# Performance work log

Hardware: AMD Instinct MI355X
Metric: run time of the kernel (lower is better)

Reference implementation:

```python
import jax, jax.numpy as jnp
import numpy as np

N_NODES = 50000
N_EDGES = 600000
IN_C = 128
HID = 128
OUT_C = 64
N_GCN = 4  # num_layers - 2
SKIP = 0.5
EPS = 1e-5


def setup_inputs() -> dict:
    key = jax.random.key(0)
    ks = jax.random.split(key, 10)
    x = jax.random.normal(ks[0], (N_NODES, IN_C), dtype=jnp.float32)
    edge_index = jax.random.randint(ks[1], (2, N_EDGES), 0, N_NODES, dtype=jnp.int64)
    s = 0.05
    W_in = jax.random.normal(ks[2], (IN_C, HID), dtype=jnp.float32) * s
    b_in = jnp.zeros((HID,), jnp.float32)
    W_g = jax.random.normal(ks[3], (N_GCN, HID, HID), dtype=jnp.float32) * s
    b_g = jnp.zeros((N_GCN, HID), jnp.float32)
    gamma = jnp.ones((N_GCN, HID), jnp.float32)
    beta = jnp.zeros((N_GCN, HID), jnp.float32)
    W_out = jax.random.normal(ks[4], (HID, OUT_C), dtype=jnp.float32) * s
    b_out = jnp.zeros((OUT_C,), jnp.float32)
    return {"x": x, "W_in": W_in, "b_in": b_in, "W_g": W_g, "b_g": b_g,
            "gamma": gamma, "beta": beta, "W_out": W_out, "b_out": b_out,
            "edge_index": edge_index}


def _forward(x, W_in, b_in, W_g, b_g, gamma, beta, W_out, b_out, edge_index):
    n = x.shape[0]
    src, dst = edge_index[0], edge_index[1]
    # GCN symmetric normalization with self-loops: deg = in-degree + 1
    deg = jnp.zeros((n,), x.dtype).at[dst].add(1.0) + 1.0
    dis = jax.lax.rsqrt(deg)  # deg >= 1 thanks to self-loops
    enorm = dis[src] * dis[dst]        # [E] per-edge norm
    self_norm = dis * dis              # [N] self-loop norm

    h = x @ W_in + b_in                # convs[0]: Linear in->hidden
    x_skip = h
    acc = jnp.zeros_like(h)
    for i in range(W_g.shape[0]):      # GCNConv layers (original i = 1..num_layers-2)
        t = h @ W_g[i]                 # [N, HID]
        agg = jax.ops.segment_sum(t[src] * enorm[:, None], dst, num_segments=n)
        agg = agg + t * self_norm[:, None] + b_g[i]  # self-loops + GCNConv bias
        # BatchNorm1d (training-mode batch stats, biased variance)
        mean = agg.mean(axis=0)
        var = jnp.mean((agg - mean) ** 2, axis=0)
        t = (agg - mean) * jax.lax.rsqrt(var + EPS) * gamma[i] + beta[i]
        if (i + 1) % 2 == 0:           # original: if i % 2 == 0 with i starting at 1
            t = t + SKIP * x_skip
        h = jax.nn.relu(t)             # dropout = identity (eval mode)
        acc = acc + h
    return acc @ W_out + b_out         # convs[-1]: Linear hidden->out


def reference(x, W_in, b_in, W_g, b_g, gamma, beta, W_out, b_out, edge_index):
    return _forward(x, W_in, b_in, W_g, b_g, gamma, beta, W_out, b_out, edge_index)
```

## Files before the change

kernel.cpp:

```cpp
#include <hip/hip_runtime.h>

using short8  = __attribute__((ext_vector_type(8))) short;
using floatx4 = __attribute__((ext_vector_type(4))) float;

static __device__ __forceinline__ float bf2f(unsigned short u) {
    union { unsigned u; float f; } v; v.u = ((unsigned)u) << 16; return v.f;
}
static __device__ __forceinline__ unsigned short f2bf(float f) {
    union { float f; unsigned u; } v; v.f = f;
    unsigned r = v.u + 0x7FFFu + ((v.u >> 16) & 1u);
    return (unsigned short)(r >> 16);
}

__global__ void histw_kernel(const int* __restrict__ dst, int* __restrict__ cnt, int E,
                             const float* __restrict__ Win, const float* __restrict__ Wg,
                             const float* __restrict__ Wout,
                             unsigned short* __restrict__ WinT, unsigned short* __restrict__ WgT,
                             unsigned short* __restrict__ WoutT) {
    int HB = (E + 255) >> 8;
    int b = blockIdx.x;
    if (b < HB) {
        int i = b * 256 + threadIdx.x;
        if (i < E) atomicAdd(&cnt[dst[i]], 1);
    } else {
        int i = (b - HB) * 256 + threadIdx.x;
        if (i < 16384) {
            int m = i & 127, k = i >> 7;
            WinT[m * 128 + k] = f2bf(Win[i]);
        } else if (i < 81920) {
            int j = i - 16384;
            int m = j & 127, k = (j >> 7) & 127, mat = j >> 14;
            WgT[mat * 16384 + m * 128 + k] = f2bf(Wg[j]);
        } else if (i < 90112) {
            int j = i - 81920;
            int m = j % 64, k = j / 64;
            WoutT[m * 128 + k] = f2bf(Wout[j]);
        }
    }
}

__global__ __launch_bounds__(256) void scanall_kernel(const int* __restrict__ cnt,
        unsigned* __restrict__ bsum, unsigned* __restrict__ boff, unsigned* __restrict__ done,
        int* __restrict__ rowptr, int* __restrict__ cursor,
        float* __restrict__ dis, float* __restrict__ selfn, int n, int nb) {
    __shared__ int s[256];
    __shared__ int s2[256];
    __shared__ int flag_agg;
    __shared__ int blkoff;
    const int b = blockIdx.x, tid = threadIdx.x;
    int i = b * 256 + tid;
    int cc = (i < n) ? cnt[i] : 0;
    s[tid] = cc;
    __syncthreads();
    for (int off = 1; off < 256; off <<= 1) {
        int t = s[tid];
        int a = (tid >= off) ? s[tid - off] : 0;
        __syncthreads();
        s[tid] = t + a;
        __syncthreads();
    }
    if (tid == 0) {
        atomicExch(&bsum[b], (unsigned)s[255] | 0x80000000u);
        __threadfence();
        unsigned t = atomicAdd(done, 1u);
        flag_agg = (t == (unsigned)(nb - 1)) ? 1 : 0;
    }
    __syncthreads();
    if (flag_agg) {
        __threadfence();
        unsigned val = (tid < nb) ? (atomicOr(&bsum[tid], 0u) & 0x7fffffffu) : 0u;
        s2[tid] = (int)val;
        __syncthreads();
        for (int off = 1; off < 256; off <<= 1) {
            int t = s2[tid];
            int a = (tid >= off) ? s2[tid - off] : 0;
            __syncthreads();
            s2[tid] = t + a;
            __syncthreads();
        }
        if (tid < nb)
            atomicExch(&boff[tid], ((unsigned)s2[tid] - val) | 0x80000000u);
    }
    if (tid == 0) {
        unsigned vv;
        while (((vv = atomicOr(&boff[b], 0u)) & 0x80000000u) == 0u)
            __builtin_amdgcn_s_sleep(8);
        blkoff = (int)(vv & 0x7fffffffu);
    }
    __syncthreads();
    if (i < n) {
        int pre = blkoff + s[tid] - cc;
        rowptr[i] = pre;
        cursor[i] = pre;
        float d = (float)cc + 1.0f;
        dis[i] = rsqrtf(d);
        selfn[i] = 1.0f / d;
        if (i == n - 1) rowptr[n] = pre + cc;
    }
}

__global__ __launch_bounds__(256) void fillgemm_kernel(
        const float* __restrict__ X,
        const unsigned short* __restrict__ W1T, const float* __restrict__ b1,
        const unsigned short* __restrict__ W2T,
        unsigned short* __restrict__ H0, unsigned short* __restrict__ T0, int nrows, int GB,
        const int* __restrict__ src, const int* __restrict__ dst,
        int* __restrict__ cursor, const float* __restrict__ dis,
        unsigned long long* __restrict__ epack, int E) {
    __shared__ unsigned short Al[64 * 136];
    __shared__ unsigned short Wl[128 * 136];
    const int tid = threadIdx.x;

    if (blockIdx.x >= GB) {
        int i = (blockIdx.x - GB) * 256 + tid;
        if (i < E) {
            int s = src[i], d = dst[i];
            int p = atomicAdd(&cursor[d], 1);
            float w = dis[s] * dis[d];
            unsigned long long rec = (unsigned long long)(unsigned)s |
                                     ((unsigned long long)__float_as_uint(w) << 32);
            __builtin_nontemporal_store(rec, &epack[p]);
        }
        return;
    }

    const int w     = tid >> 6;
    const int lane  = tid & 63;
    const int col_l = lane & 15;
    const int quad  = lane >> 4;
    const int row_base = blockIdx.x * 64;

#pragma unroll
    for (int it = 0; it < 8; ++it) {
        int idx = it * 256 + tid;
        int r = idx >> 5, c4 = idx & 31;
        int gr = row_base + r; if (gr >= nrows) gr = nrows - 1;
        float4 v = *(const float4*)&X[(size_t)gr * 128 + c4 * 4];
        ushort4 u;
        u.x = f2bf(v.x); u.y = f2bf(v.y); u.z = f2bf(v.z); u.w = f2bf(v.w);
        *(ushort4*)&Al[r * 136 + c4 * 4] = u;
    }
#pragma unroll
    for (int it = 0; it < 8; ++it) {
        int idx = it * 256 + tid;
        int r = idx >> 4, ch = idx & 15;
        *(float4*)&Wl[r * 136 + ch * 8] = *(const float4*)&W1T[(size_t)r * 128 + ch * 8];
    }
    __syncthreads();

    short8 af[4];
    const int arow = w * 16 + col_l;
#pragma unroll
    for (int ks = 0; ks < 4; ++ks)
        af[ks] = *(const short8*)&Al[arow * 136 + ks * 32 + quad * 8];

    floatx4 acc[8];
#pragma unroll
    for (int ct = 0; ct < 8; ++ct) {
        acc[ct] = (floatx4){0.f, 0.f, 0.f, 0.f};
#pragma unroll
        for (int ks = 0; ks < 4; ++ks) {
            short8 bf = *(const short8*)&Wl[(ct * 16 + col_l) * 136 + ks * 32 + quad * 8];
            acc[ct] = __builtin_amdgcn_mfma_f32_16x16x32_bf16(af[ks], bf, acc[ct], 0, 0, 0);
        }
    }
    __syncthreads();

#pragma unroll
    for (int ct = 0; ct < 8; ++ct) {
        int col = ct * 16 + col_l;
        float bv = b1[col];
#pragma unroll
        for (int r = 0; r < 4; ++r) {
            int row_l = w * 16 + quad * 4 + r;
            float o = acc[ct][r] + bv;
            unsigned short ob = f2bf(o);
            Al[row_l * 136 + col] = ob;
            int gr = row_base + row_l;
            if (gr < nrows) H0[(size_t)gr * 128 + col] = ob;
        }
    }
#pragma unroll
    for (int it = 0; it < 8; ++it) {
        int idx = it * 256 + tid;
        int r = idx >> 4, ch = idx & 15;
        *(float4*)&Wl[r * 136 + ch * 8] = *(const float4*)&W2T[(size_t)r * 128 + ch * 8];
    }
    __syncthreads();

#pragma unroll
    for (int ks = 0; ks < 4; ++ks)
        af[ks] = *(const short8*)&Al[arow * 136 + ks * 32 + quad * 8];
#pragma unroll
    for (int ct = 0; ct < 8; ++ct) {
        acc[ct] = (floatx4){0.f, 0.f, 0.f, 0.f};
#pragma unroll
        for (int ks = 0; ks < 4; ++ks) {
            short8 bf = *(const short8*)&Wl[(ct * 16 + col_l) * 136 + ks * 32 + quad * 8];
            acc[ct] = __builtin_amdgcn_mfma_f32_16x16x32_bf16(af[ks], bf, acc[ct], 0, 0, 0);
        }
    }
#pragma unroll
    for (int ct = 0; ct < 8; ++ct) {
        int col = ct * 16 + col_l;
#pragma unroll
        for (int r = 0; r < 4; ++r) {
            int gr = row_base + w * 16 + quad * 4 + r;
            if (gr < nrows) T0[(size_t)gr * 128 + col] = f2bf(acc[ct][r]);
        }
    }
}

template<int MO, bool STAGE_ACC, bool OB16>
__global__ __launch_bounds__(256) void mgemm_bn_kernel(
        const unsigned short* __restrict__ AGGB, const float* __restrict__ stats,
        const float* __restrict__ gamma, const float* __restrict__ beta,
        const unsigned short* __restrict__ XSKIP, unsigned short* __restrict__ ACC,
        const unsigned short* __restrict__ WT, const float* __restrict__ bias,
        void* __restrict__ C, int nrows, float inv_n, int do_skip, int first) {
    constexpr int NT = MO / 16;
    __shared__ unsigned short Al[64 * 136];
    __shared__ unsigned short Wl[MO * 136];
    __shared__ float ABl[256];
    const int tid   = threadIdx.x;
    const int w     = tid >> 6;
    const int lane  = tid & 63;
    const int col_l = lane & 15;
    const int quad  = lane >> 4;
    const int row_base = blockIdx.x * 64;

    if (tid < 128) {
        float s = 0.f, ss = 0.f;
#pragma unroll
        for (int k = 0; k < 8; ++k) {
            s  += stats[k * 256 + tid];
            ss += stats[k * 256 + 128 + tid];
        }
        float m = s * inv_n;
        float var = ss * inv_n - m * m;
        float inv = rsqrtf(var + 1e-5f);
        float Ax = inv * gamma[tid];
        ABl[tid] = Ax;
        ABl[128 + tid] = beta[tid] - m * Ax;
    }
#pragma unroll
    for (int it = 0; it < MO / 16; ++it) {
        int idx = it * 256 + tid;
        int r = idx >> 4, ch = idx & 15;
        *(float4*)&Wl[r * 136 + ch * 8] = *(const float4*)&WT[(size_t)r * 128 + ch * 8];
    }
    __syncthreads();

#pragma unroll
    for (int it = 0; it < 8; ++it) {
        int idx = it * 256 + tid;
        int r = idx >> 5, c4 = idx & 31;
        int gr = row_base + r;
        ushort4 hu = make_ushort4(0, 0, 0, 0);
        if (gr < nrows) {
            ushort4 xb = *(const ushort4*)&AGGB[(size_t)gr * 128 + c4 * 4];
            float4 Av = ((const float4*)ABl)[c4];
            float4 Bv = ((const float4*)ABl)[32 + c4];
            float4 t;
            t.x = fmaf(bf2f(xb.x), Av.x, Bv.x);
            t.y = fmaf(bf2f(xb.y), Av.y, Bv.y);
            t.z = fmaf(bf2f(xb.z), Av.z, Bv.z);
            t.w = fmaf(bf2f(xb.w), Av.w, Bv.w);
            if (do_skip) {
                ushort4 sk = *(const ushort4*)&XSKIP[(size_t)gr * 128 + c4 * 4];
                t.x = fmaf(0.5f, bf2f(sk.x), t.x);
                t.y = fmaf(0.5f, bf2f(sk.y), t.y);
                t.z = fmaf(0.5f, bf2f(sk.z), t.z);
                t.w = fmaf(0.5f, bf2f(sk.w), t.w);
            }
            t.x = fmaxf(t.x, 0.f); t.y = fmaxf(t.y, 0.f);
            t.z = fmaxf(t.z, 0.f); t.w = fmaxf(t.w, 0.f);
            float4 a;
            if (first) {
                a = t;
            } else {
                ushort4 ab = *(const ushort4*)&ACC[(size_t)gr * 128 + c4 * 4];
                a.x = bf2f(ab.x) + t.x;
                a.y = bf2f(ab.y) + t.y;
                a.z = bf2f(ab.z) + t.z;
                a.w = bf2f(ab.w) + t.w;
            }
            float4 sv;
            if (STAGE_ACC) sv = a; else sv = t;
            hu.x = f2bf(sv.x); hu.y = f2bf(sv.y); hu.z = f2bf(sv.z); hu.w = f2bf(sv.w);
            if (!STAGE_ACC) {
                ushort4 au;
                au.x = f2bf(a.x); au.y = f2bf(a.y); au.z = f2bf(a.z); au.w = f2bf(a.w);
                *(ushort4*)&ACC[(size_t)gr * 128 + c4 * 4] = au;
            }
        }
        *(ushort4*)&Al[r * 136 + c4 * 4] = hu;
    }
    __syncthreads();

    short8 af[4];
    const int arow = w * 16 + col_l;
#pragma unroll
    for (int ks = 0; ks < 4; ++ks)
        af[ks] = *(const short8*)&Al[arow * 136 + ks * 32 + quad * 8];

    floatx4 acc[NT];
#pragma unroll
    for (int ct = 0; ct < NT; ++ct) {
        acc[ct] = (floatx4){0.f, 0.f, 0.f, 0.f};
#pragma unroll
        for (int ks = 0; ks < 4; ++ks) {
            short8 bf = *(const short8*)&Wl[(ct * 16 + col_l) * 136 + ks * 32 + quad * 8];
            acc[ct] = __builtin_amdgcn_mfma_f32_16x16x32_bf16(af[ks], bf, acc[ct], 0, 0, 0);
        }
    }

#pragma unroll
    for (int ct = 0; ct < NT; ++ct) {
        int col = ct * 16 + col_l;
        float bv = bias ? bias[col] : 0.f;
#pragma unroll
        for (int r = 0; r < 4; ++r) {
            int gr = row_base + w * 16 + quad * 4 + r;
            if (gr < nrows) {
                float o = acc[ct][r] + bv;
                if (OB16) ((unsigned short*)C)[(size_t)gr * MO + col] = f2bf(o);
                else      ((float*)C)[(size_t)gr * MO + col] = o;
            }
        }
    }
}

__global__ __launch_bounds__(256) void aggstat_kernel(const unsigned short* __restrict__ T,
        const int* __restrict__ rowptr, const unsigned long long* __restrict__ epack,
        const float* __restrict__ selfn,
        unsigned short* __restrict__ AGGB, float* __restrict__ stats, int n, int nw) {
    const int w    = threadIdx.x >> 6;
    const int lane = threadIdx.x & 63;
    const int wid  = blockIdx.x * 4 + w;
    const int c    = lane * 2;
    float s1x = 0.f, s1y = 0.f, s2x = 0.f, s2y = 0.f;

    for (int v = wid; v < n; v += nw) {
        ushort2 tv = *(const ushort2*)&T[(size_t)v * 128 + c];
        float sn = selfn[v];
        float ax = bf2f(tv.x) * sn, ay = bf2f(tv.y) * sn;
        int e = rowptr[v], e1 = rowptr[v + 1];
        for (; e + 8 <= e1; e += 8) {
            unsigned long long d[8]; ushort2 t[8];
#pragma unroll
            for (int j = 0; j < 8; ++j) d[j] = __builtin_nontemporal_load(&epack[e + j]);
#pragma unroll
            for (int j = 0; j < 8; ++j)
                t[j] = *(const ushort2*)&T[(size_t)(unsigned)d[j] * 128 + c];
#pragma unroll
            for (int j = 0; j < 8; ++j) {
                float wj = __uint_as_float((unsigned)(d[j] >> 32));
                ax = fmaf(wj, bf2f(t[j].x), ax);
                ay = fmaf(wj, bf2f(t[j].y), ay);
            }
        }
        for (; e + 4 <= e1; e += 4) {
            unsigned long long d[4]; ushort2 t[4];
#pragma unroll
            for (int j = 0; j < 4; ++j) d[j] = __builtin_nontemporal_load(&epack[e + j]);
#pragma unroll
            for (int j = 0; j < 4; ++j)
                t[j] = *(const ushort2*)&T[(size_t)(unsigned)d[j] * 128 + c];
#pragma unroll
            for (int j = 0; j < 4; ++j) {
                float wj = __uint_as_float((unsigned)(d[j] >> 32));
                ax = fmaf(wj, bf2f(t[j].x), ax);
                ay = fmaf(wj, bf2f(t[j].y), ay);
            }
        }
        for (; e < e1; ++e) {
            unsigned long long d0 = __builtin_nontemporal_load(&epack[e]);
            ushort2 tu = *(const ushort2*)&T[(size_t)(unsigned)d0 * 128 + c];
            float w0 = __uint_as_float((unsigned)(d0 >> 32));
            ax = fmaf(w0, bf2f(tu.x), ax);
            ay = fmaf(w0, bf2f(tu.y), ay);
        }
        ushort2 o; o.x = f2bf(ax); o.y = f2bf(ay);
        *(ushort2*)&AGGB[(size_t)v * 128 + c] = o;
        float rx = bf2f(o.x), ry = bf2f(o.y);
        s1x += rx; s1y += ry;
        s2x = fmaf(rx, rx, s2x); s2y = fmaf(ry, ry, s2y);
    }

    __shared__ float r1[4][130];
    __shared__ float r2[4][130];
    r1[w][c] = s1x; r1[w][c + 1] = s1y;
    r2[w][c] = s2x; r2[w][c + 1] = s2y;
    __syncthreads();
    if (w == 0) {
        float a1 = r1[0][c] + r1[1][c] + r1[2][c] + r1[3][c];
        float b1 = r1[0][c + 1] + r1[1][c + 1] + r1[2][c + 1] + r1[3][c + 1];
        float a2 = r2[0][c] + r2[1][c] + r2[2][c] + r2[3][c];
        float b2 = r2[0][c + 1] + r2[1][c + 1] + r2[2][c + 1] + r2[3][c + 1];
        float* sh = stats + (blockIdx.x & 7) * 256;
        atomicAdd(&sh[c], a1);
        atomicAdd(&sh[c + 1], b1);
        atomicAdd(&sh[128 + c], a2);
        atomicAdd(&sh[128 + c + 1], b2);
    }
}

extern "C" void kernel_launch(void* const* d_in, const int* in_sizes, int n_in,
                              void* d_out, int out_size, void* d_ws, size_t ws_size,
                              hipStream_t stream) {
    (void)n_in; (void)out_size; (void)ws_size;
    const float* x    = (const float*)d_in[0];
    const float* Win  = (const float*)d_in[1];
    const float* bin  = (const float*)d_in[2];
    const float* Wg   = (const float*)d_in[3];
    const float* gamma = (const float*)d_in[5];
    const float* beta  = (const float*)d_in[6];
    const float* Wout  = (const float*)d_in[7];
    const float* bout  = (const float*)d_in[8];
    const int*   eidx  = (const int*)d_in[9];
    float* out = (float*)d_out;

    const int N = in_sizes[0] / 128;
    const int E = in_sizes[9] / 2;
    const int* esrc_in = eidx;
    const int* edst_in = eidx + E;

    char* p = (char*)d_ws;
    auto alloc = [&](size_t bytes) { char* r = p; p += (bytes + 255) & ~(size_t)255; return r; };
    const size_t NB2 = (size_t)N * 128 * sizeof(unsigned short);
    unsigned short* h0b   = (unsigned short*)alloc(NB2);
    unsigned short* tb16  = (unsigned short*)alloc(NB2);
    unsigned short* aggb  = (unsigned short*)alloc(NB2);
    unsigned short* accb  = (unsigned short*)alloc(NB2);
    unsigned short* WinT  = (unsigned short*)alloc(128 * 128 * 2);
    unsigned short* WgT   = (unsigned short*)alloc(4 * 128 * 128 * 2);
    unsigned short* WoutT = (unsigned short*)alloc(128 * 64 * 2);
    float* disb  = (float*)alloc((size_t)N * 4);
    float* selfn = (float*)alloc((size_t)N * 4);
    char* z0 = p;
    int*      cnt    = (int*)alloc((size_t)N * 4);
    unsigned* bsum   = (unsigned*)alloc(256 * 4);
    unsigned* boff   = (unsigned*)alloc(256 * 4);
    unsigned* done   = (unsigned*)alloc(256);
    float*    stats4 = (float*)alloc((size_t)4 * 8 * 256 * 4);
    const size_t zbytes = (size_t)(p - z0);
    int*   rowptr = (int*)alloc((size_t)(N + 1) * 4);
    int*   cursor = (int*)alloc((size_t)N * 4);
    unsigned long long* epack = (unsigned long long*)alloc((size_t)E * 8);

    auto cdiv = [](int a, int b) { return (a + b - 1) / b; };
    const int NBLK = cdiv(N, 256);
    const float inv_n = 1.0f / (float)N;
    const int AGG_BLOCKS = 2048;
    const int AGG_WAVES  = AGG_BLOCKS * 4;
    const int GB = cdiv(N, 64);
    const int FB = cdiv(E, 256);

    hipMemsetAsync(z0, 0, zbytes, stream);
    histw_kernel<<<cdiv(E, 256) + 352, 256, 0, stream>>>(edst_in, cnt, E,
                                                         Win, Wg, Wout, WinT, WgT, WoutT);
    scanall_kernel<<<NBLK, 256, 0, stream>>>(cnt, bsum, boff, done, rowptr, cursor,
                                             disb, selfn, N, NBLK);

    fillgemm_kernel<<<GB + FB, 256, 0, stream>>>(x, WinT, bin, WgT, h0b, tb16, N, GB,
                                                 esrc_in, edst_in, cursor, disb, epack, E);

    for (int i = 0; i < 4; ++i) {
        float* stats = stats4 + (size_t)i * 8 * 256;
        aggstat_kernel<<<AGG_BLOCKS, 256, 0, stream>>>(tb16, rowptr, epack, selfn,
                                                       aggb, stats, N, AGG_WAVES);
        if (i < 3) {
            mgemm_bn_kernel<128, false, true><<<cdiv(N, 64), 256, 0, stream>>>(
                aggb, stats, gamma + i * 128, beta + i * 128, h0b, accb,
                WgT + (size_t)(i + 1) * 128 * 128, nullptr, (void*)tb16, N,
                inv_n, (i & 1), (i == 0) ? 1 : 0);
        } else {
            mgemm_bn_kernel<64, true, false><<<cdiv(N, 64), 256, 0, stream>>>(
                aggb, stats, gamma + i * 128, beta + i * 128, h0b, accb,
                WoutT, bout, (void*)out, N, inv_n, 1, 0);
        }
    }
}
```

Measured before the change: 417.4 us.

## Build CSR edge list via two-level bucketed staging with shared-memory atomics

```diff
diff --git a/kernel.cpp b/kernel.cpp
--- a/kernel.cpp
+++ b/kernel.cpp
@@ -41,7 +41,7 @@
 
 __global__ __launch_bounds__(256) void scanall_kernel(const int* __restrict__ cnt,
         unsigned* __restrict__ bsum, unsigned* __restrict__ boff, unsigned* __restrict__ done,
-        int* __restrict__ rowptr, int* __restrict__ cursor,
+        int* __restrict__ rowptr,
         float* __restrict__ dis, float* __restrict__ selfn, int n, int nb) {
     __shared__ int s[256];
     __shared__ int s2[256];
@@ -91,7 +91,6 @@
     if (i < n) {
         int pre = blkoff + s[tid] - cc;
         rowptr[i] = pre;
-        cursor[i] = pre;
         float d = (float)cc + 1.0f;
         dis[i] = rsqrtf(d);
         selfn[i] = 1.0f / d;
@@ -105,21 +104,21 @@
         const unsigned short* __restrict__ W2T,
         unsigned short* __restrict__ H0, unsigned short* __restrict__ T0, int nrows, int GB,
         const int* __restrict__ src, const int* __restrict__ dst,
-        int* __restrict__ cursor, const float* __restrict__ dis,
-        unsigned long long* __restrict__ epack, int E) {
+        int* __restrict__ cursor8, unsigned* __restrict__ stage, int E) {
     __shared__ unsigned short Al[64 * 136];
     __shared__ unsigned short Wl[128 * 136];
     const int tid = threadIdx.x;
 
     if (blockIdx.x >= GB) {
-        int i = (blockIdx.x - GB) * 256 + tid;
+        int k = blockIdx.x - GB;
+        int i = k * 256 + tid;
         if (i < E) {
             int s = src[i], d = dst[i];
-            int p = atomicAdd(&cursor[d], 1);
-            float w = dis[s] * dis[d];
-            unsigned long long rec = (unsigned long long)(unsigned)s |
-                                     ((unsigned long long)__float_as_uint(w) << 32);
-            __builtin_nontemporal_store(rec, &epack[p]);
+            int bk = (d >> 8) * 8 + (k & 7);
+            int idx = atomicAdd(&cursor8[bk], 1);
+            if (idx > 1023) idx = 1023;
+            unsigned rec = (unsigned)s | ((unsigned)(d & 255) << 16);
+            __builtin_nontemporal_store(rec, &stage[(unsigned)bk * 1024 + idx]);
         }
         return;
     }
@@ -207,6 +206,35 @@
         for (int r = 0; r < 4; ++r) {
             int gr = row_base + w * 16 + quad * 4 + r;
             if (gr < nrows) T0[(size_t)gr * 128 + col] = f2bf(acc[ct][r]);
+        }
+    }
+}
+
+__global__ __launch_bounds__(256) void scatter_kernel(
+        const unsigned* __restrict__ stage, const int* __restrict__ cursor8,
+        const int* __restrict__ rowptr, const float* __restrict__ dis,
+        unsigned long long* __restrict__ epack, int n) {
+    __shared__ int   curs[256];
+    __shared__ float disn[256];
+    const int b = blockIdx.x, tid = threadIdx.x;
+    int node = b * 256 + tid;
+    if (node < n) { curs[tid] = rowptr[node]; disn[tid] = dis[node]; }
+    else          { curs[tid] = 0;            disn[tid] = 0.f; }
+    __syncthreads();
+#pragma unroll 1
+    for (int s = 0; s < 8; ++s) {
+        int bk  = b * 8 + s;
+        int cnt = cursor8[bk]; if (cnt > 1024) cnt = 1024;
+        const unsigned* sg = stage + (unsigned)bk * 1024;
+        for (int i = tid; i < cnt; i += 256) {
+            unsigned rec = sg[i];
+            int sc = rec & 0xFFFF;
+            int dl = (rec >> 16) & 255;
+            int slot = atomicAdd(&curs[dl], 1);
+            float w = dis[sc] * disn[dl];
+            unsigned long long r2 = (unsigned long long)(unsigned)sc |
+                                    ((unsigned long long)__float_as_uint(w) << 32);
+            epack[slot] = r2;
         }
     }
 }
@@ -438,15 +466,18 @@
     unsigned short* WoutT = (unsigned short*)alloc(128 * 64 * 2);
     float* disb  = (float*)alloc((size_t)N * 4);
     float* selfn = (float*)alloc((size_t)N * 4);
+
+    const int NBUK = (N + 255) / 256;
     char* z0 = p;
     int*      cnt    = (int*)alloc((size_t)N * 4);
     unsigned* bsum   = (unsigned*)alloc(256 * 4);
     unsigned* boff   = (unsigned*)alloc(256 * 4);
     unsigned* done   = (unsigned*)alloc(256);
     float*    stats4 = (float*)alloc((size_t)4 * 8 * 256 * 4);
+    int*      cursor8 = (int*)alloc((size_t)NBUK * 8 * 4);
     const size_t zbytes = (size_t)(p - z0);
-    int*   rowptr = (int*)alloc((size_t)(N + 1) * 4);
-    int*   cursor = (int*)alloc((size_t)N * 4);
+    int*      rowptr = (int*)alloc((size_t)(N + 1) * 4);
+    unsigned* stage  = (unsigned*)alloc((size_t)NBUK * 8 * 1024 * 4);
     unsigned long long* epack = (unsigned long long*)alloc((size_t)E * 8);
 
     auto cdiv = [](int a, int b) { return (a + b - 1) / b; };
@@ -460,11 +491,12 @@
     hipMemsetAsync(z0, 0, zbytes, stream);
     histw_kernel<<<cdiv(E, 256) + 352, 256, 0, stream>>>(edst_in, cnt, E,
                                                          Win, Wg, Wout, WinT, WgT, WoutT);
-    scanall_kernel<<<NBLK, 256, 0, stream>>>(cnt, bsum, boff, done, rowptr, cursor,
+    scanall_kernel<<<NBLK, 256, 0, stream>>>(cnt, bsum, boff, done, rowptr,
                                              disb, selfn, N, NBLK);
 
     fillgemm_kernel<<<GB + FB, 256, 0, stream>>>(x, WinT, bin, WgT, h0b, tb16, N, GB,
-                                                 esrc_in, edst_in, cursor, disb, epack, E);
+                                                 esrc_in, edst_in, cursor8, stage, E);
+    scatter_kernel<<<NBUK, 256, 0, stream>>>(stage, cursor8, rowptr, disb, epack, N);
 
     for (int i = 0; i < 4; ++i) {
         float* stats = stats4 + (size_t)i * 8 * 256;
```

New measurement: 503.8 us. +20.7%, slower.

## Fuse histogram and scan into one kernel with a grid-wide barrier

Applied to the files above, without the earlier changes.

```diff
diff --git a/kernel.cpp b/kernel.cpp
--- a/kernel.cpp
+++ b/kernel.cpp
@@ -12,18 +12,19 @@
     return (unsigned short)(r >> 16);
 }
 
-__global__ void histw_kernel(const int* __restrict__ dst, int* __restrict__ cnt, int E,
-                             const float* __restrict__ Win, const float* __restrict__ Wg,
-                             const float* __restrict__ Wout,
-                             unsigned short* __restrict__ WinT, unsigned short* __restrict__ WgT,
-                             unsigned short* __restrict__ WoutT) {
-    int HB = (E + 255) >> 8;
-    int b = blockIdx.x;
-    if (b < HB) {
-        int i = b * 256 + threadIdx.x;
-        if (i < E) atomicAdd(&cnt[dst[i]], 1);
-    } else {
-        int i = (b - HB) * 256 + threadIdx.x;
+__global__ __launch_bounds__(256) void histscan_kernel(
+        const int* __restrict__ dst, int* __restrict__ cnt, int E,
+        const float* __restrict__ Win, const float* __restrict__ Wg,
+        const float* __restrict__ Wout,
+        unsigned short* __restrict__ WinT, unsigned short* __restrict__ WgT,
+        unsigned short* __restrict__ WoutT,
+        unsigned* __restrict__ bsum, unsigned* __restrict__ boff, unsigned* __restrict__ done,
+        int* __restrict__ rowptr,
+        float* __restrict__ dis, float* __restrict__ selfn, int n, int nb) {
+    const int b = blockIdx.x, tid = threadIdx.x;
+    const int stride = nb * 256;
+
+    for (int i = b * 256 + tid; i < 90112; i += stride) {
         if (i < 16384) {
             int m = i & 127, k = i >> 7;
             WinT[m * 128 + k] = f2bf(Win[i]);
@@ -31,25 +32,30 @@
             int j = i - 16384;
             int m = j & 127, k = (j >> 7) & 127, mat = j >> 14;
             WgT[mat * 16384 + m * 128 + k] = f2bf(Wg[j]);
-        } else if (i < 90112) {
+        } else {
             int j = i - 81920;
             int m = j % 64, k = j / 64;
             WoutT[m * 128 + k] = f2bf(Wout[j]);
         }
     }
-}
-
-__global__ __launch_bounds__(256) void scanall_kernel(const int* __restrict__ cnt,
-        unsigned* __restrict__ bsum, unsigned* __restrict__ boff, unsigned* __restrict__ done,
-        int* __restrict__ rowptr, int* __restrict__ cursor,
-        float* __restrict__ dis, float* __restrict__ selfn, int n, int nb) {
+    for (int i = b * 256 + tid; i < E; i += stride)
+        atomicAdd(&cnt[dst[i]], 1);
+
+    __syncthreads();
+    if (tid == 0) {
+        __threadfence();
+        atomicAdd(&done[0], 1u);
+        while (atomicOr(&done[0], 0u) < (unsigned)nb)
+            __builtin_amdgcn_s_sleep(8);
+    }
+    __syncthreads();
+
     __shared__ int s[256];
     __shared__ int s2[256];
     __shared__ int flag_agg;
     __shared__ int blkoff;
-    const int b = blockIdx.x, tid = threadIdx.x;
     int i = b * 256 + tid;
-    int cc = (i < n) ? cnt[i] : 0;
+    int cc = (i < n) ? (int)atomicOr((unsigned*)&cnt[i], 0u) : 0;
     s[tid] = cc;
     __syncthreads();
     for (int off = 1; off < 256; off <<= 1) {
@@ -62,7 +68,7 @@
     if (tid == 0) {
         atomicExch(&bsum[b], (unsigned)s[255] | 0x80000000u);
         __threadfence();
-        unsigned t = atomicAdd(done, 1u);
+        unsigned t = atomicAdd(&done[1], 1u);
         flag_agg = (t == (unsigned)(nb - 1)) ? 1 : 0;
     }
     __syncthreads();
@@ -91,7 +97,6 @@
     if (i < n) {
         int pre = blkoff + s[tid] - cc;
         rowptr[i] = pre;
-        cursor[i] = pre;
         float d = (float)cc + 1.0f;
         dis[i] = rsqrtf(d);
         selfn[i] = 1.0f / d;
@@ -349,7 +354,7 @@
         for (; e + 8 <= e1; e += 8) {
             unsigned long long d[8]; ushort2 t[8];
 #pragma unroll
-            for (int j = 0; j < 8; ++j) d[j] = __builtin_nontemporal_load(&epack[e + j]);
+            for (int j = 0; j < 8; ++j) d[j] = epack[e + j];
 #pragma unroll
             for (int j = 0; j < 8; ++j)
                 t[j] = *(const ushort2*)&T[(size_t)(unsigned)d[j] * 128 + c];
@@ -363,7 +368,7 @@
         for (; e + 4 <= e1; e += 4) {
             unsigned long long d[4]; ushort2 t[4];
 #pragma unroll
-            for (int j = 0; j < 4; ++j) d[j] = __builtin_nontemporal_load(&epack[e + j]);
+            for (int j = 0; j < 4; ++j) d[j] = epack[e + j];
 #pragma unroll
             for (int j = 0; j < 4; ++j)
                 t[j] = *(const ushort2*)&T[(size_t)(unsigned)d[j] * 128 + c];
@@ -375,7 +380,7 @@
             }
         }
         for (; e < e1; ++e) {
-            unsigned long long d0 = __builtin_nontemporal_load(&epack[e]);
+            unsigned long long d0 = epack[e];
             ushort2 tu = *(const ushort2*)&T[(size_t)(unsigned)d0 * 128 + c];
             float w0 = __uint_as_float((unsigned)(d0 >> 32));
             ax = fmaf(w0, bf2f(tu.x), ax);
@@ -458,10 +463,11 @@
     const int FB = cdiv(E, 256);
 
     hipMemsetAsync(z0, 0, zbytes, stream);
-    histw_kernel<<<cdiv(E, 256) + 352, 256, 0, stream>>>(edst_in, cnt, E,
-                                                         Win, Wg, Wout, WinT, WgT, WoutT);
-    scanall_kernel<<<NBLK, 256, 0, stream>>>(cnt, bsum, boff, done, rowptr, cursor,
-                                             disb, selfn, N, NBLK);
+    histscan_kernel<<<NBLK, 256, 0, stream>>>(edst_in, cnt, E,
+                                              Win, Wg, Wout, WinT, WgT, WoutT,
+                                              bsum, boff, done, rowptr,
+                                              disb, selfn, N, NBLK);
+    hipMemcpyAsync(cursor, rowptr, (size_t)N * 4, hipMemcpyDeviceToDevice, stream);
 
     fillgemm_kernel<<<GB + FB, 256, 0, stream>>>(x, WinT, bin, WgT, h0b, tb16, N, GB,
                                                  esrc_in, edst_in, cursor, disb, epack, E);
```

New measurement: 418.1 us. Within noise of the previous version (+0.2%).
